# Performance work log

Measured on AMD Instinct MI355X. Metric: run time of the kernel, lower is better.

## Reference

```python
import jax, jax.numpy as jnp
import numpy as np

N_HEAD = 12

def setup_inputs() -> dict:
    key = jax.random.key(0)
    k1, k2, k3 = jax.random.split(key, 3)
    B, T, C = 8, 1024, 768
    x = jax.random.normal(k1, (B, T, C), dtype=jnp.float32)
    # Linear weights stored as [in, out] so y = x @ W + b (same math as torch Linear)
    w_attn = jax.random.normal(k2, (C, 3 * C), dtype=jnp.float32) * (1.0 / np.sqrt(C))
    b_attn = jnp.zeros((3 * C,), dtype=jnp.float32)
    w_proj = jax.random.normal(k3, (C, C), dtype=jnp.float32) * (1.0 / np.sqrt(C))
    b_proj = jnp.zeros((C,), dtype=jnp.float32)
    return {"x": x, "w_attn": w_attn, "b_attn": b_attn, "w_proj": w_proj, "b_proj": b_proj}

def reference(x, w_attn, b_attn, w_proj, b_proj):
    B, T, C = x.shape
    H = N_HEAD
    D = C // H
    qkv = x @ w_attn + b_attn                        # [B,T,3C]
    q, k, v = jnp.split(qkv, 3, axis=-1)             # each [B,T,C]
    q = q.reshape(B, T, H, D).transpose(0, 2, 1, 3)  # [B,H,T,D]
    k = k.reshape(B, T, H, D).transpose(0, 2, 1, 3)
    v = v.reshape(B, T, H, D).transpose(0, 2, 1, 3)
    scale = 1.0 / jnp.sqrt(jnp.asarray(D, dtype=x.dtype))
    att = jnp.einsum('bhqd,bhkd->bhqk', q, k) * scale  # [B,H,T,T]
    causal = jnp.tril(jnp.ones((T, T), dtype=bool))    # [T,T]
    att = jnp.where(causal[None, None], att, jnp.asarray(-jnp.inf, dtype=att.dtype))
    att = jax.nn.softmax(att, axis=-1)
    out = jnp.einsum('bhqk,bhkd->bhqd', att, v)        # [B,H,T,D]
    out = out.transpose(0, 2, 1, 3).reshape(B, T, C)
    return out @ w_proj + b_proj
```

## Files before the change

kernel.cpp:

```cpp
#include <hip/hip_runtime.h>
#include <hip/hip_bf16.h>
#include <cmath>

#define B_ 8
#define T_ 1024
#define C_ 768
#define H_ 12
#define D_ 64
#define N3C 2304
#define M_ 8192

typedef __bf16 bf16x8 __attribute__((ext_vector_type(8)));
typedef float  f32x4  __attribute__((ext_vector_type(4)));

typedef const __attribute__((address_space(1))) void* gptr_t;
typedef __attribute__((address_space(3))) void* lptr_t;

#define LOG2E 1.44269504088896f

__device__ __forceinline__ bf16x8 cvt_bf16x8(const float4& a, const float4& b) {
    bf16x8 r;
    r[0] = (__bf16)a.x; r[1] = (__bf16)a.y; r[2] = (__bf16)a.z; r[3] = (__bf16)a.w;
    r[4] = (__bf16)b.x; r[5] = (__bf16)b.y; r[6] = (__bf16)b.z; r[7] = (__bf16)b.w;
    return r;
}

__global__ __launch_bounds__(256) void prepass(const float* __restrict__ x,
                                               __bf16* __restrict__ xb,
                                               const float* __restrict__ wa,
                                               __bf16* __restrict__ wat,
                                               const float* __restrict__ wp,
                                               __bf16* __restrict__ wpt) {
    __shared__ float tile[32][33];
    const int bx = blockIdx.x, tid = threadIdx.x;
    if (bx < 3072) {
        int i = (bx * 256 + tid) * 8;
        float4 a = *(const float4*)&x[i];
        float4 b = *(const float4*)&x[i + 4];
        *(bf16x8*)&xb[i] = cvt_bf16x8(a, b);
        return;
    }
    const float* w;
    __bf16* wt;
    int K, N, n0, k0;
    if (bx < 4800) {
        int bb = bx - 3072;
        w = wa; wt = wat; K = 768; N = 2304;
        n0 = (bb % 72) * 32; k0 = (bb / 72) * 32;
    } else {
        int bb = bx - 4800;
        w = wp; wt = wpt; K = 768; N = 768;
        n0 = (bb % 24) * 32; k0 = (bb / 24) * 32;
    }
    int tx = tid & 31, ty = tid >> 5;
#pragma unroll
    for (int i = 0; i < 4; i++)
        tile[ty + i * 8][tx] = w[(size_t)(k0 + ty + i * 8) * N + n0 + tx];
    __syncthreads();
#pragma unroll
    for (int i = 0; i < 4; i++)
        wt[(size_t)(n0 + ty + i * 8) * K + k0 + tx] = (__bf16)tile[tx][ty + i * 8];
}

__global__ __launch_bounds__(256) void qkv_gemm_mfma(const __bf16* __restrict__ A,
                                                     const __bf16* __restrict__ Bt,
                                                     const float* __restrict__ bias,
                                                     __bf16* __restrict__ qb,
                                                     __bf16* __restrict__ kb,
                                                     __bf16* __restrict__ vbt) {
    __shared__ __bf16 smem[128 * 136];
    __bf16* As = smem;
    __bf16* Bs = smem + 128 * 64;
    const int tid = threadIdx.x;
    const int wave = tid >> 6, lane = tid & 63;
    const int lane15 = lane & 15, quad = lane >> 4;
    const int m0 = blockIdx.y * 128, n0 = blockIdx.x * 128;
    const int wm = (wave >> 1) * 64, wn = (wave & 1) * 64;
    f32x4 acc[4][4] = {};

    for (int k0 = 0; k0 < 768; k0 += 64) {
#pragma unroll
        for (int r = 0; r < 4; ++r) {
            int p = r * 256 + tid;
            int mrow = p >> 3, csw = p & 7;
            int ksrc = (csw ^ (mrow & 7)) * 8;
            __builtin_amdgcn_global_load_lds(
                (gptr_t)(A + (size_t)(m0 + mrow) * 768 + k0 + ksrc),
                (lptr_t)(As + (r * 256 + wave * 64) * 8), 16, 0, 0);
            __builtin_amdgcn_global_load_lds(
                (gptr_t)(Bt + (size_t)(n0 + mrow) * 768 + k0 + ksrc),
                (lptr_t)(Bs + (r * 256 + wave * 64) * 8), 16, 0, 0);
        }
        __syncthreads();
#pragma unroll
        for (int ks = 0; ks < 2; ++ks) {
            bf16x8 af[4], bf[4];
#pragma unroll
            for (int mt = 0; mt < 4; ++mt) {
                int m = wm + mt * 16 + lane15;
                int csw = (ks * 4 + quad) ^ (m & 7);
                af[mt] = *(const bf16x8*)(As + m * 64 + csw * 8);
            }
#pragma unroll
            for (int nt = 0; nt < 4; ++nt) {
                int n = wn + nt * 16 + lane15;
                int csw = (ks * 4 + quad) ^ (n & 7);
                bf[nt] = *(const bf16x8*)(Bs + n * 64 + csw * 8);
            }
#pragma unroll
            for (int mt = 0; mt < 4; ++mt)
#pragma unroll
                for (int nt = 0; nt < 4; ++nt)
                    acc[mt][nt] = __builtin_amdgcn_mfma_f32_16x16x32_bf16(af[mt], bf[nt], acc[mt][nt], 0, 0, 0);
        }
        __syncthreads();
    }

    if (n0 < 1536) {
        const bool isq = (n0 < 768);
        const float sc = isq ? (0.125f * LOG2E) : 1.0f;
#pragma unroll
        for (int nt = 0; nt < 4; ++nt) {
            int n = n0 + wn + nt * 16 + lane15;
            int rem = isq ? n : (n - 768);
            int h = rem >> 6;
            int d = n & 63;
            float bv = bias[n];
            __bf16* dst = isq ? qb : kb;
#pragma unroll
            for (int mt = 0; mt < 4; ++mt) {
#pragma unroll
                for (int reg = 0; reg < 4; ++reg) {
                    int mrow = m0 + wm + mt * 16 + quad * 4 + reg;
                    int bb = mrow >> 10, t = mrow & 1023;
                    dst[(((size_t)bb * H_ + h) * T_ + t) * D_ + d] =
                        (__bf16)((acc[mt][nt][reg] + bv) * sc);
                }
            }
        }
    } else {
        __bf16* vls = smem;
#pragma unroll
        for (int nt = 0; nt < 4; ++nt) {
            int nl = wn + nt * 16 + lane15;
            float bv = bias[n0 + nl];
#pragma unroll
            for (int mt = 0; mt < 4; ++mt)
#pragma unroll
                for (int reg = 0; reg < 4; ++reg)
                    vls[nl * 136 + wm + mt * 16 + quad * 4 + reg] =
                        (__bf16)(acc[mt][nt][reg] + bv);
        }
        __syncthreads();
        int nl = tid >> 1;
        int t0 = (tid & 1) * 64;
        int n = n0 + nl;
        int h = (n - 1536) >> 6;
        int d = n & 63;
        int bb = m0 >> 10, tg = (m0 & 1023) + t0;
        __bf16* dst = vbt + (((size_t)bb * H_ + h) * D_ + d) * T_ + tg;
        const __bf16* srcl = vls + nl * 136 + t0;
#pragma unroll
        for (int c = 0; c < 8; ++c)
            *(bf16x8*)(dst + c * 8) = *(const bf16x8*)(srcl + c * 8);
    }
}

__global__ __launch_bounds__(256) void proj_gemm_mfma(const __bf16* __restrict__ A,
                                                      const __bf16* __restrict__ Bt,
                                                      const float* __restrict__ bias,
                                                      float* __restrict__ out) {
    __shared__ __bf16 As[128 * 64];
    __shared__ __bf16 Bs[64 * 64];
    const int tid = threadIdx.x;
    const int wave = tid >> 6, lane = tid & 63;
    const int lane15 = lane & 15, quad = lane >> 4;
    const int m0 = blockIdx.y * 128, n0 = blockIdx.x * 64;
    const int wm = wave * 32;
    f32x4 acc[2][4] = {};

    for (int k0 = 0; k0 < 768; k0 += 64) {
#pragma unroll
        for (int r = 0; r < 4; ++r) {
            int p = r * 256 + tid;
            int mrow = p >> 3, csw = p & 7;
            int ksrc = (csw ^ (mrow & 7)) * 8;
            __builtin_amdgcn_global_load_lds(
                (gptr_t)(A + (size_t)(m0 + mrow) * 768 + k0 + ksrc),
                (lptr_t)(As + (r * 256 + wave * 64) * 8), 16, 0, 0);
        }
#pragma unroll
        for (int r = 0; r < 2; ++r) {
            int p = r * 256 + tid;
            int nrow = p >> 3, csw = p & 7;
            int ksrc = (csw ^ (nrow & 7)) * 8;
            __builtin_amdgcn_global_load_lds(
                (gptr_t)(Bt + (size_t)(n0 + nrow) * 768 + k0 + ksrc),
                (lptr_t)(Bs + (r * 256 + wave * 64) * 8), 16, 0, 0);
        }
        __syncthreads();
#pragma unroll
        for (int ks = 0; ks < 2; ++ks) {
            bf16x8 af[2], bf[4];
#pragma unroll
            for (int mt = 0; mt < 2; ++mt) {
                int m = wm + mt * 16 + lane15;
                int csw = (ks * 4 + quad) ^ (m & 7);
                af[mt] = *(const bf16x8*)(As + m * 64 + csw * 8);
            }
#pragma unroll
            for (int nt = 0; nt < 4; ++nt) {
                int n = nt * 16 + lane15;
                int csw = (ks * 4 + quad) ^ (n & 7);
                bf[nt] = *(const bf16x8*)(Bs + n * 64 + csw * 8);
            }
#pragma unroll
            for (int mt = 0; mt < 2; ++mt)
#pragma unroll
                for (int nt = 0; nt < 4; ++nt)
                    acc[mt][nt] = __builtin_amdgcn_mfma_f32_16x16x32_bf16(af[mt], bf[nt], acc[mt][nt], 0, 0, 0);
        }
        __syncthreads();
    }

#pragma unroll
    for (int nt = 0; nt < 4; ++nt) {
        int n = n0 + nt * 16 + lane15;
        float bv = bias[n];
#pragma unroll
        for (int mt = 0; mt < 2; ++mt) {
#pragma unroll
            for (int reg = 0; reg < 4; ++reg) {
                int mrow = m0 + wm + mt * 16 + quad * 4 + reg;
                out[(size_t)mrow * C_ + n] = acc[mt][nt][reg] + bv;
            }
        }
    }
}

__global__ __launch_bounds__(256) void attn_mfma(const __bf16* __restrict__ qb,
                                                 const __bf16* __restrict__ kb,
                                                 const __bf16* __restrict__ vbt,
                                                 __bf16* __restrict__ ao) {
    __shared__ __bf16 Ks[2][64 * 64];
    __shared__ __bf16 Vts[2][64 * 64];
    __shared__ __bf16 Ps[4 * 32 * 72];

    const int tid = threadIdx.x;
    const int wave = tid >> 6, lane = tid & 63;
    const int lane15 = lane & 15, quad = lane >> 4;
    const int bh = blockIdx.x;
    const int qt = 7 - blockIdx.y;
    const int b = bh / H_, h = bh % H_;
    const int q0 = qt * 128;

    const __bf16* Kb = kb + (size_t)bh * T_ * D_;
    const __bf16* Vb = vbt + (size_t)bh * D_ * T_;
    __bf16* Pw = Ps + wave * 32 * 72;

    bf16x8 qf[2][2];
#pragma unroll
    for (int g = 0; g < 2; ++g) {
        const __bf16* qrow = qb + ((size_t)bh * T_ + q0 + wave * 32 + g * 16 + lane15) * D_ + quad * 8;
        qf[g][0] = *(const bf16x8*)qrow;
        qf[g][1] = *(const bf16x8*)(qrow + 32);
    }

    f32x4 o[2][4] = {};
    float lsum[2][4] = {};

    const int kunits = 2 * qt + 2;

#define STAGE(KU, BUF)                                                             \
    {                                                                              \
        const int k0s = (KU) * 64;                                                 \
        _Pragma("unroll")                                                          \
        for (int r = 0; r < 2; ++r) {                                              \
            int p = r * 256 + tid;                                                 \
            int row = p >> 3, c = p & 7;                                           \
            int cs = (c ^ (row & 7)) * 8;                                          \
            __builtin_amdgcn_global_load_lds(                                      \
                (gptr_t)(Kb + (size_t)(k0s + row) * D_ + cs),                      \
                (lptr_t)(&Ks[BUF][0] + (r * 256 + wave * 64) * 8), 16, 0, 0);      \
            __builtin_amdgcn_global_load_lds(                                      \
                (gptr_t)(Vb + (size_t)row * T_ + k0s + cs),                        \
                (lptr_t)(&Vts[BUF][0] + (r * 256 + wave * 64) * 8), 16, 0, 0);     \
        }                                                                          \
    }

    STAGE(0, 0);

    for (int ku = 0; ku < kunits; ++ku) {
        __syncthreads();
        if (ku + 1 < kunits) STAGE(ku + 1, (ku + 1) & 1);
        const __bf16* Kc = &Ks[ku & 1][0];
        const __bf16* Vc = &Vts[ku & 1][0];
        const int k0 = ku * 64;

        f32x4 s[2][4];
#pragma unroll
        for (int kt = 0; kt < 4; ++kt) {
            int row = kt * 16 + lane15;
            bf16x8 kf0 = *(const bf16x8*)(Kc + row * 64 + ((quad) ^ (row & 7)) * 8);
            bf16x8 kf1 = *(const bf16x8*)(Kc + row * 64 + ((4 + quad) ^ (row & 7)) * 8);
#pragma unroll
            for (int g = 0; g < 2; ++g) {
                f32x4 t = {};
                t = __builtin_amdgcn_mfma_f32_16x16x32_bf16(qf[g][0], kf0, t, 0, 0, 0);
                t = __builtin_amdgcn_mfma_f32_16x16x32_bf16(qf[g][1], kf1, t, 0, 0, 0);
                s[g][kt] = t;
            }
        }

        const bool diag = (ku >= 2 * qt);
#pragma unroll
        for (int g = 0; g < 2; ++g) {
#pragma unroll
            for (int kt = 0; kt < 4; ++kt) {
                int col = k0 + kt * 16 + lane15;
#pragma unroll
                for (int r = 0; r < 4; ++r) {
                    float p = __builtin_amdgcn_exp2f(s[g][kt][r]);
                    if (diag) {
                        int qrow = q0 + wave * 32 + g * 16 + quad * 4 + r;
                        if (col > qrow) p = 0.f;
                    }
                    lsum[g][r] += p;
                    Pw[(g * 16 + quad * 4 + r) * 72 + kt * 16 + lane15] = (__bf16)p;
                }
            }
        }

        bf16x8 vf[4][2];
#pragma unroll
        for (int dt = 0; dt < 4; ++dt) {
            int row = dt * 16 + lane15;
#pragma unroll
            for (int half = 0; half < 2; ++half)
                vf[dt][half] = *(const bf16x8*)(Vc + row * 64 + ((half * 4 + quad) ^ (row & 7)) * 8);
        }
#pragma unroll
        for (int g = 0; g < 2; ++g) {
#pragma unroll
            for (int half = 0; half < 2; ++half) {
                bf16x8 pf = *(const bf16x8*)(Pw + (g * 16 + lane15) * 72 + half * 32 + quad * 8);
#pragma unroll
                for (int dt = 0; dt < 4; ++dt)
                    o[g][dt] = __builtin_amdgcn_mfma_f32_16x16x32_bf16(pf, vf[dt][half], o[g][dt], 0, 0, 0);
            }
        }
    }

#pragma unroll
    for (int g = 0; g < 2; ++g) {
        float inv[4];
#pragma unroll
        for (int r = 0; r < 4; ++r) {
            float ls = lsum[g][r];
            ls += __shfl_xor(ls, 1);
            ls += __shfl_xor(ls, 2);
            ls += __shfl_xor(ls, 4);
            ls += __shfl_xor(ls, 8);
            inv[r] = 1.0f / ls;
        }
#pragma unroll
        for (int dt = 0; dt < 4; ++dt) {
#pragma unroll
            for (int r = 0; r < 4; ++r) {
                int t = q0 + wave * 32 + g * 16 + quad * 4 + r;
                ao[((size_t)(b * T_ + t)) * C_ + h * 64 + dt * 16 + lane15] =
                    (__bf16)(o[g][dt][r] * inv[r]);
            }
        }
    }
}

extern "C" void kernel_launch(void* const* d_in, const int* in_sizes, int n_in,
                              void* d_out, int out_size, void* d_ws, size_t ws_size,
                              hipStream_t stream) {
    const float* x = (const float*)d_in[0];
    const float* w_attn = (const float*)d_in[1];
    const float* b_attn = (const float*)d_in[2];
    const float* w_proj = (const float*)d_in[3];
    const float* b_proj = (const float*)d_in[4];
    float* out = (float*)d_out;

    __bf16* xb = (__bf16*)d_ws;
    __bf16* wat = xb + (size_t)M_ * C_;
    __bf16* wpt = wat + (size_t)N3C * C_;
    __bf16* qb = wpt + (size_t)C_ * C_;
    __bf16* kb = qb + (size_t)96 * T_ * D_;
    __bf16* vbt = kb + (size_t)96 * T_ * D_;
    __bf16* ao = vbt + (size_t)96 * T_ * D_;

    prepass<<<5376, 256, 0, stream>>>(x, xb, w_attn, wat, w_proj, wpt);
    qkv_gemm_mfma<<<dim3(N3C / 128, M_ / 128), 256, 0, stream>>>(xb, wat, b_attn, qb, kb, vbt);
    attn_mfma<<<dim3(96, 8), 256, 0, stream>>>(qb, kb, vbt, ao);
    proj_gemm_mfma<<<dim3(C_ / 64, M_ / 128), 256, 0, stream>>>(ao, wpt, b_proj, out);
}
```

Before: 194.8 us.

## Register-prefetch GEMM tiles and remap blocks to share weight tiles across XCDs

Both GEMM kernels drop the direct global-to-LDS loads in favour of a register double-buffer. The next K-tile is loaded into registers while the current tile is consumed by MFMA, and one barrier per iteration is removed. Launches become 1D, and the block index is remapped so consecutive blocks walk different M rows under the same N column, aiming for better L2 reuse across chiplets. The cost is extra VGPR pressure and explicit LDS store instructions in place of the asynchronous LDS-load path.

```diff
diff --git a/kernel.cpp b/kernel.cpp
--- a/kernel.cpp
+++ b/kernel.cpp
@@ -74,22 +74,42 @@
     const int tid = threadIdx.x;
     const int wave = tid >> 6, lane = tid & 63;
     const int lane15 = lane & 15, quad = lane >> 4;
-    const int m0 = blockIdx.y * 128, n0 = blockIdx.x * 128;
+    const int bid = blockIdx.x;
+    const int m0 = ((bid & 7) * 8 + ((bid >> 3) & 7)) * 128;
+    const int n0 = (bid >> 6) * 128;
     const int wm = (wave >> 1) * 64, wn = (wave & 1) * 64;
     f32x4 acc[4][4] = {};
 
+    int mrow[4], ksrc[4];
+#pragma unroll
+    for (int r = 0; r < 4; ++r) {
+        int p = r * 256 + tid;
+        mrow[r] = p >> 3;
+        ksrc[r] = ((p & 7) ^ (mrow[r] & 7)) * 8;
+    }
+
+    float4 ra[4], rb[4];
+#pragma unroll
+    for (int r = 0; r < 4; ++r) {
+        ra[r] = *(const float4*)(A + (size_t)(m0 + mrow[r]) * 768 + ksrc[r]);
+        rb[r] = *(const float4*)(Bt + (size_t)(n0 + mrow[r]) * 768 + ksrc[r]);
+    }
+
     for (int k0 = 0; k0 < 768; k0 += 64) {
+        if (k0) __syncthreads();
 #pragma unroll
         for (int r = 0; r < 4; ++r) {
             int p = r * 256 + tid;
-            int mrow = p >> 3, csw = p & 7;
-            int ksrc = (csw ^ (mrow & 7)) * 8;
-            __builtin_amdgcn_global_load_lds(
-                (gptr_t)(A + (size_t)(m0 + mrow) * 768 + k0 + ksrc),
-                (lptr_t)(As + (r * 256 + wave * 64) * 8), 16, 0, 0);
-            __builtin_amdgcn_global_load_lds(
-                (gptr_t)(Bt + (size_t)(n0 + mrow) * 768 + k0 + ksrc),
-                (lptr_t)(Bs + (r * 256 + wave * 64) * 8), 16, 0, 0);
+            *(float4*)(As + p * 8) = ra[r];
+            *(float4*)(Bs + p * 8) = rb[r];
+        }
+        if (k0 + 64 < 768) {
+            int kn = k0 + 64;
+#pragma unroll
+            for (int r = 0; r < 4; ++r) {
+                ra[r] = *(const float4*)(A + (size_t)(m0 + mrow[r]) * 768 + kn + ksrc[r]);
+                rb[r] = *(const float4*)(Bt + (size_t)(n0 + mrow[r]) * 768 + kn + ksrc[r]);
+            }
         }
         __syncthreads();
 #pragma unroll
@@ -113,8 +133,8 @@
                 for (int nt = 0; nt < 4; ++nt)
                     acc[mt][nt] = __builtin_amdgcn_mfma_f32_16x16x32_bf16(af[mt], bf[nt], acc[mt][nt], 0, 0, 0);
         }
-        __syncthreads();
-    }
+    }
+    __syncthreads();
 
     if (n0 < 1536) {
         const bool isq = (n0 < 768);
@@ -131,8 +151,8 @@
             for (int mt = 0; mt < 4; ++mt) {
 #pragma unroll
                 for (int reg = 0; reg < 4; ++reg) {
-                    int mrow = m0 + wm + mt * 16 + quad * 4 + reg;
-                    int bb = mrow >> 10, t = mrow & 1023;
+                    int mr = m0 + wm + mt * 16 + quad * 4 + reg;
+                    int bb = mr >> 10, t = mr & 1023;
                     dst[(((size_t)bb * H_ + h) * T_ + t) * D_ + d] =
                         (__bf16)((acc[mt][nt][reg] + bv) * sc);
                 }
@@ -175,28 +195,44 @@
     const int tid = threadIdx.x;
     const int wave = tid >> 6, lane = tid & 63;
     const int lane15 = lane & 15, quad = lane >> 4;
-    const int m0 = blockIdx.y * 128, n0 = blockIdx.x * 64;
+    const int bid = blockIdx.x;
+    const int m0 = ((bid & 7) * 8 + ((bid >> 3) & 7)) * 128;
+    const int n0 = (bid >> 6) * 64;
     const int wm = wave * 32;
     f32x4 acc[2][4] = {};
 
+    int mrow[4], ksrc[4];
+#pragma unroll
+    for (int r = 0; r < 4; ++r) {
+        int p = r * 256 + tid;
+        mrow[r] = p >> 3;
+        ksrc[r] = ((p & 7) ^ (mrow[r] & 7)) * 8;
+    }
+
+    float4 ra[4], rb[2];
+#pragma unroll
+    for (int r = 0; r < 4; ++r)
+        ra[r] = *(const float4*)(A + (size_t)(m0 + mrow[r]) * 768 + ksrc[r]);
+#pragma unroll
+    for (int r = 0; r < 2; ++r)
+        rb[r] = *(const float4*)(Bt + (size_t)(n0 + mrow[r]) * 768 + ksrc[r]);
+
     for (int k0 = 0; k0 < 768; k0 += 64) {
-#pragma unroll
-        for (int r = 0; r < 4; ++r) {
-            int p = r * 256 + tid;
-            int mrow = p >> 3, csw = p & 7;
-            int ksrc = (csw ^ (mrow & 7)) * 8;
-            __builtin_amdgcn_global_load_lds(
-                (gptr_t)(A + (size_t)(m0 + mrow) * 768 + k0 + ksrc),
-                (lptr_t)(As + (r * 256 + wave * 64) * 8), 16, 0, 0);
-        }
-#pragma unroll
-        for (int r = 0; r < 2; ++r) {
-            int p = r * 256 + tid;
-            int nrow = p >> 3, csw = p & 7;
-            int ksrc = (csw ^ (nrow & 7)) * 8;
-            __builtin_amdgcn_global_load_lds(
-                (gptr_t)(Bt + (size_t)(n0 + nrow) * 768 + k0 + ksrc),
-                (lptr_t)(Bs + (r * 256 + wave * 64) * 8), 16, 0, 0);
+        if (k0) __syncthreads();
+#pragma unroll
+        for (int r = 0; r < 4; ++r)
+            *(float4*)(As + (r * 256 + tid) * 8) = ra[r];
+#pragma unroll
+        for (int r = 0; r < 2; ++r)
+            *(float4*)(Bs + (r * 256 + tid) * 8) = rb[r];
+        if (k0 + 64 < 768) {
+            int kn = k0 + 64;
+#pragma unroll
+            for (int r = 0; r < 4; ++r)
+                ra[r] = *(const float4*)(A + (size_t)(m0 + mrow[r]) * 768 + kn + ksrc[r]);
+#pragma unroll
+            for (int r = 0; r < 2; ++r)
+                rb[r] = *(const float4*)(Bt + (size_t)(n0 + mrow[r]) * 768 + kn + ksrc[r]);
         }
         __syncthreads();
 #pragma unroll
@@ -220,7 +256,6 @@
                 for (int nt = 0; nt < 4; ++nt)
                     acc[mt][nt] = __builtin_amdgcn_mfma_f32_16x16x32_bf16(af[mt], bf[nt], acc[mt][nt], 0, 0, 0);
         }
-        __syncthreads();
     }
 
 #pragma unroll
@@ -231,8 +266,8 @@
         for (int mt = 0; mt < 2; ++mt) {
 #pragma unroll
             for (int reg = 0; reg < 4; ++reg) {
-                int mrow = m0 + wm + mt * 16 + quad * 4 + reg;
-                out[(size_t)mrow * C_ + n] = acc[mt][nt][reg] + bv;
+                int mr = m0 + wm + mt * 16 + quad * 4 + reg;
+                out[(size_t)mr * C_ + n] = acc[mt][nt][reg] + bv;
             }
         }
     }
@@ -394,7 +429,7 @@
     __bf16* ao = vbt + (size_t)96 * T_ * D_;
 
     prepass<<<5376, 256, 0, stream>>>(x, xb, w_attn, wat, w_proj, wpt);
-    qkv_gemm_mfma<<<dim3(N3C / 128, M_ / 128), 256, 0, stream>>>(xb, wat, b_attn, qb, kb, vbt);
+    qkv_gemm_mfma<<<1152, 256, 0, stream>>>(xb, wat, b_attn, qb, kb, vbt);
     attn_mfma<<<dim3(96, 8), 256, 0, stream>>>(qb, kb, vbt, ao);
-    proj_gemm_mfma<<<dim3(C_ / 64, M_ / 128), 256, 0, stream>>>(ao, wpt, b_proj, out);
-}
+    proj_gemm_mfma<<<768, 256, 0, stream>>>(ao, wpt, b_proj, out);
+}
```

Result: slower. 308.1 us (+58.2%).
